# Kernel optimization log

Measured on AMD Instinct MI355X. Metric: run time of the kernel, lower is better.

Reference implementation:

```python
import jax, jax.numpy as jnp
import numpy as np

B, S, D, H = 2, 2048, 4096, 32
Dh = D // H          # 128, rotary_dim == head_dim
BASE = 10000.0       # rope_theta
SCALE = Dh ** -0.5


def setup_inputs() -> dict:
    key = jax.random.key(0)
    k0, k1, k2 = jax.random.split(key, 3)
    w_scale = 0.02
    return {
        "hidden_states": jax.random.normal(k0, (B, S, D), jnp.float32),
        "positions": jnp.broadcast_to(jnp.arange(S, dtype=jnp.int32), (B, S)),
        "Wqkv": jax.random.normal(k1, (D, 3 * D), jnp.float32) * w_scale,
        "bqkv": jnp.zeros((3 * D,), jnp.float32),
        "Wproj": jax.random.normal(k2, (D, D), jnp.float32) * w_scale,
    }


def _apply_rope(x, positions):
    # x: [B, S, H, Dh]; neox-style (rotate-half) RoPE, as in vLLM PagedAttentionWithRoPE
    half = Dh // 2
    inv_freq = 1.0 / (BASE ** (jnp.arange(half, dtype=jnp.float32) / half))
    ang = positions[..., None].astype(jnp.float32) * inv_freq      # [B, S, half]
    cos = jnp.cos(ang)[:, :, None, :]                              # [B, S, 1, half]
    sin = jnp.sin(ang)[:, :, None, :]
    x1, x2 = x[..., :half], x[..., half:]
    return jnp.concatenate([x1 * cos - x2 * sin, x2 * cos + x1 * sin], axis=-1)


def reference(hidden_states, positions, Wqkv, bqkv, Wproj):
    # c_attn: fused QKV projection
    qkv = hidden_states @ Wqkv + bqkv                              # [B, S, 3D]
    q, k, v = jnp.split(qkv, 3, axis=-1)
    q = q.reshape(B, S, H, Dh)
    k = k.reshape(B, S, H, Dh)
    v = v.reshape(B, S, H, Dh)
    # fused RoPE on q and k at the given positions
    q = _apply_rope(q, positions)
    k = _apply_rope(k, positions)
    # causal scaled-dot-product attention (prefill semantics of paged attention)
    scores = jnp.einsum("bqhd,bkhd->bhqk", q, k) * SCALE           # [B, H, S, S]
    causal = jnp.tril(jnp.ones((S, S), dtype=bool))
    scores = jnp.where(causal, scores, jnp.finfo(scores.dtype).min)
    attn = jax.nn.softmax(scores, axis=-1)
    ctx = jnp.einsum("bhqk,bkhd->bqhd", attn, v).reshape(B, S, D)
    # c_proj (no bias)
    return ctx @ Wproj
```

## Files before the change

kernel.cpp:

```cpp
#include <hip/hip_runtime.h>

typedef __attribute__((ext_vector_type(8))) short short8;
typedef __attribute__((ext_vector_type(4))) short short4v;
typedef __attribute__((ext_vector_type(4))) float f32x4;

#define LDS8(base, off) (*(const short8*)((const char*)(base) + (off)))
#define GLOAD_LDS16(gp, lp) __builtin_amdgcn_global_load_lds( \
    (const __attribute__((address_space(1))) unsigned int*)(gp), \
    (__attribute__((address_space(3))) unsigned int*)(lp), 16, 0, 0)
#define SBAR() __builtin_amdgcn_s_barrier()
#define SB0() __builtin_amdgcn_sched_barrier(0)

__device__ __forceinline__ short f2bf(float f) {
    unsigned u = __builtin_bit_cast(unsigned, f);
    unsigned r = (u + 0x7FFFu + ((u >> 16) & 1u)) >> 16;
    return (short)r;
}
__device__ __forceinline__ float bf2f(short s) {
    unsigned u = ((unsigned)(unsigned short)s) << 16;
    return __builtin_bit_cast(float, u);
}

__global__ __launch_bounds__(256) void cvt_f32_bf16(const float* __restrict__ in,
                                                    short* __restrict__ out, int n8) {
    int i = blockIdx.x * 256 + threadIdx.x;
    if (i < n8) {
        const f32x4* p = (const f32x4*)(in + (size_t)i * 8);
        f32x4 a = p[0], bq = p[1];
        short8 o;
        o[0] = f2bf(a[0]); o[1] = f2bf(a[1]); o[2] = f2bf(a[2]); o[3] = f2bf(a[3]);
        o[4] = f2bf(bq[0]); o[5] = f2bf(bq[1]); o[6] = f2bf(bq[2]); o[7] = f2bf(bq[3]);
        *(short8*)(out + (size_t)i * 8) = o;
    }
}

__global__ __launch_bounds__(256) void transpose_cvt(const float* __restrict__ W,
                                                     short* __restrict__ Out, int R, int C,
                                                     int permqk) {
    __shared__ float tile[64][33];
    int c0 = blockIdx.x * 64, r0 = blockIdx.y * 32;
    int tid = threadIdx.x;
    int cc4 = (tid & 15) * 4;
#pragma unroll
    for (int it = 0; it < 2; ++it) {
        int rr = (tid >> 4) + it * 16;
        f32x4 v = *(const f32x4*)&W[(size_t)(r0 + rr) * C + c0 + cc4];
#pragma unroll
        for (int i = 0; i < 4; ++i) tile[cc4 + i][rr] = v[i];
    }
    __syncthreads();
    int cc = tid >> 2, r8 = (tid & 3) * 8;
    short8 o;
#pragma unroll
    for (int i = 0; i < 8; ++i) o[i] = f2bf(tile[cc][r8 + i]);
    int orow = c0 + cc;
    if (permqk && orow < 8192) {
        int j = orow & 127;
        int jp = (j < 64) ? (j << 1) : (((j - 64) << 1) | 1);
        orow = (orow & ~127) | jp;
    }
    *(short8*)&Out[(size_t)orow * R + r0 + r8] = o;
}

__global__ __launch_bounds__(256) void rope_table(float* __restrict__ ctab, float* __restrict__ stab) {
    int idx = blockIdx.x * 256 + threadIdx.x;
    int t = idx >> 6, j = idx & 63;
    float inv = expf(-(float)j * (9.210340371976184f / 64.0f));
    float ang = (float)t * inv;
    ctab[idx] = cosf(ang);
    stab[idx] = sinf(ang);
}

__global__ __launch_bounds__(512, 2) void gemm256(const short* __restrict__ A,
                                                  const short* __restrict__ Bt,
                                                  const float* __restrict__ bias,
                                                  float* __restrict__ Cf,
                                                  int M, int N, int K, int nN,
                                                  const int* __restrict__ pos,
                                                  const float* __restrict__ ctab,
                                                  const float* __restrict__ stab,
                                                  short* __restrict__ Qr,
                                                  short* __restrict__ Kr,
                                                  short* __restrict__ Vtt,
                                                  int mode) {
    __shared__ __align__(16) char smem[131072];
    const int tid = threadIdx.x;
    const int l = tid & 63, w = tid >> 6;
    const int m = l & 15, g = l >> 4, m7 = m & 7;
    const int wm = w >> 2, wn = w & 3;

    int cpx = gridDim.x >> 3;
    int wg = (blockIdx.x & 7) * cpx + (blockIdx.x >> 3);
    int gsz = nN << 3;
    int grp = wg / gsz, rem = wg - grp * gsz;
    int bm = (grp << 3) + (rem & 7);
    int bn = rem >> 3;
    int m0 = bm << 8, n0 = bn << 8;

    const int srow = l >> 3;
    const int sgcol = ((l & 7) ^ srow) << 3;
    const int NT = K >> 6;

    const int AbaseR = wm << 14;
    const int BbaseR = 32768 + ((wn >> 1) << 14);
    const int brow0 = (wn & 1) << 6;

    f32x4 acc[8][4];
    const f32x4 fz = {0.f, 0.f, 0.f, 0.f};
#pragma unroll
    for (int i = 0; i < 8; ++i)
#pragma unroll
        for (int j = 0; j < 4; ++j) acc[i][j] = fz;

    auto stage_half = [&](const short* G, int grow0, int kcol, int ldsoff) {
        GLOAD_LDS16(G + (size_t)(grow0 +      w * 8 + srow) * K + kcol + sgcol,
                    smem + ldsoff + w * 1024);
        GLOAD_LDS16(G + (size_t)(grow0 + 64 + w * 8 + srow) * K + kcol + sgcol,
                    smem + ldsoff + 8192 + w * 1024);
    };

    short8 afX[2][2], afY[2][2], bf[4][2];

#define RD_AF(DST, BASE, I0)                                                     \
    _Pragma("unroll")                                                            \
    for (int i2 = 0; i2 < 2; ++i2) {                                             \
        _Pragma("unroll")                                                        \
        for (int kk = 0; kk < 2; ++kk)                                           \
            DST[i2][kk] = LDS8(BASE, (((I0) + i2) * 16 + m) * 128 + (((kk * 4 + g) ^ m7) << 4)); \
    }
#define RD_BF(BASE)                                                              \
    _Pragma("unroll")                                                            \
    for (int j2 = 0; j2 < 4; ++j2) {                                             \
        _Pragma("unroll")                                                        \
        for (int kk = 0; kk < 2; ++kk)                                           \
            bf[j2][kk] = LDS8(BASE, (brow0 + j2 * 16 + m) * 128 + (((kk * 4 + g) ^ m7) << 4)); \
    }
#define MFMA_IP(IP, AF)                                                          \
    do {                                                                         \
        __builtin_amdgcn_s_setprio(1);                                           \
        _Pragma("unroll")                                                        \
        for (int kk = 0; kk < 2; ++kk) {                                         \
            _Pragma("unroll")                                                    \
            for (int i2 = 0; i2 < 2; ++i2) {                                     \
                _Pragma("unroll")                                                \
                for (int j2 = 0; j2 < 4; ++j2) {                                 \
                    acc[(IP) * 2 + i2][j2] = __builtin_amdgcn_mfma_f32_16x16x32_bf16( \
                        AF[i2][kk], bf[j2][kk], acc[(IP) * 2 + i2][j2], 0, 0, 0); \
                }                                                                \
            }                                                                    \
        }                                                                        \
        __builtin_amdgcn_s_setprio(0);                                           \
    } while (0)

#pragma unroll
    for (int t = 0; t < 2; ++t) {
        int sb = t << 16;
        stage_half(A,  m0,       t * 64, sb);
        stage_half(A,  m0 + 128, t * 64, sb + 16384);
        stage_half(Bt, n0,       t * 64, sb + 32768);
        stage_half(Bt, n0 + 128, t * 64, sb + 49152);
    }
    asm volatile("s_waitcnt vmcnt(8)");
    SB0();
    SBAR();
    {
        const char* Ab0 = smem + AbaseR;
        const char* Bb0 = smem + BbaseR;
        RD_BF(Bb0);
        RD_AF(afX, Ab0, 0);
        SB0();
    }

    for (int kt = 0; kt < NT; ++kt) {
        const int slotb  = (kt & 1) << 16;
        const int slotbN = ((kt + 1) & 1) << 16;
        const char* Ab  = smem + slotb + AbaseR;
        const char* AbN = smem + slotbN + AbaseR;
        const char* BbN = smem + slotbN + BbaseR;
        const bool nx = (kt + 1) < NT;
        const bool pf = (kt + 2) < NT;
        const int kc = (kt + 2) << 6;

        RD_AF(afY, Ab, 2); SB0();
        asm volatile("s_waitcnt lgkmcnt(4)"); SB0();
        MFMA_IP(0, afX);
        RD_AF(afX, Ab, 4); SB0();
        asm volatile("s_waitcnt lgkmcnt(4)"); SB0();
        MFMA_IP(1, afY);
        RD_AF(afY, Ab, 6); SB0();
        asm volatile("s_waitcnt lgkmcnt(4)"); SB0();
        MFMA_IP(2, afX);
        asm volatile("s_waitcnt lgkmcnt(0)"); SB0();
        asm volatile("s_waitcnt vmcnt(0)"); SB0();
        SBAR();
        MFMA_IP(3, afY);
        if (nx) {
            RD_BF(BbN); SB0();
            RD_AF(afX, AbN, 0); SB0();
            if (pf) {
                stage_half(A,  m0,       kc, slotb);
                stage_half(A,  m0 + 128, kc, slotb + 16384);
                stage_half(Bt, n0,       kc, slotb + 32768);
                stage_half(Bt, n0 + 128, kc, slotb + 49152);
            }
        }
    }
#undef RD_AF
#undef RD_BF
#undef MFMA_IP

    if (mode == 0) {
#pragma unroll
        for (int i = 0; i < 8; ++i) {
#pragma unroll
            for (int j = 0; j < 4; ++j) {
#pragma unroll
                for (int r = 0; r < 4; ++r) {
                    int row = m0 + wm * 128 + i * 16 + g * 4 + r;
                    int col = n0 + wn * 64 + j * 16 + m;
                    Cf[(size_t)row * N + col] = acc[i][j][r];
                }
            }
        }
        return;
    }

    int region = n0 >> 12;
    if (region < 2) {
        short* Dst = (region == 0) ? Qr : Kr;
#pragma unroll
        for (int i = 0; i < 8; ++i) {
#pragma unroll
            for (int j = 0; j < 4; ++j) {
                int col = n0 + wn * 64 + j * 16 + m;
                int cr = col & 4095;
                int hh = cr >> 7;
                int jp = cr & 127;
                int jj = jp >> 1;
                int odd = jp & 1;
                int jo = jj + (odd ? 64 : 0);
                float bv = bias ? bias[region * 4096 + hh * 128 + jo] : 0.f;
#pragma unroll
                for (int r = 0; r < 4; ++r) {
                    int row = m0 + wm * 128 + i * 16 + g * 4 + r;
                    float v = acc[i][j][r] + bv;
                    float partner = __shfl_xor(v, 1, 64);
                    int p = pos[row];
                    float c = ctab[p * 64 + jj], si = stab[p * 64 + jj];
                    float outv = odd ? (v * c + partner * si) : (v * c - partner * si);
                    int bI = row >> 11, s = row & 2047;
                    Dst[((size_t)(bI * 32 + hh) * 2048 + s) * 128 + jo] = f2bf(outv);
                }
            }
        }
    } else {
#pragma unroll
        for (int i = 0; i < 8; ++i) {
#pragma unroll
            for (int j = 0; j < 4; ++j) {
                int col = n0 + wn * 64 + j * 16 + m;
                int cr = col & 4095;
                int hh = cr >> 7;
                int d = cr & 127;
                float bv = bias ? bias[8192 + cr] : 0.f;
                int row0 = m0 + wm * 128 + i * 16 + g * 4;
                int bI = row0 >> 11, s0 = row0 & 2047;
                short4v o4;
#pragma unroll
                for (int r = 0; r < 4; ++r) o4[r] = f2bf(acc[i][j][r] + bv);
                *(short4v*)&Vtt[((size_t)(bI * 32 + hh) * 128 + d) * 2048 + s0] = o4;
            }
        }
    }
}

__global__ __launch_bounds__(512, 4) void flash_fwd(const short* __restrict__ Q,
                                                    const short* __restrict__ Kt,
                                                    const short* __restrict__ Vt,
                                                    short* __restrict__ ctx) {
    const int S = 2048;
    const float SCALE = 0.08838834764831845f;
    __shared__ __align__(16) char smem[65536];

    int tid = threadIdx.x, l = tid & 63, w = tid >> 6;
    int m = l & 15, g = l >> 4, m7 = m & 7;
    int qg = blockIdx.x, h = blockIdx.y, b = blockIdx.z;
    int bh = b * 32 + h;
    int q0 = qg * 128 + w * 16;

    const short* Qg = Q + ((size_t)bh * S + q0) * 128;
    const short* Kg = Kt + (size_t)bh * S * 128;
    const short* Vg = Vt + (size_t)bh * 128 * S;

    short8 qf[4];
#pragma unroll
    for (int kb = 0; kb < 4; ++kb)
        qf[kb] = *(const short8*)(Qg + m * 128 + kb * 32 + g * 8);

    const f32x4 fz = {0.f, 0.f, 0.f, 0.f};
    f32x4 O[8];
#pragma unroll
    for (int nb = 0; nb < 8; ++nb) O[nb] = fz;
    f32x4 La = fz;
    short8 ones;
#pragma unroll
    for (int i = 0; i < 8; ++i) ones[i] = (short)0x3F80;

    const short* Kp[2]; const short* Vp[2]; int KlO[2], VlO[2];
#pragma unroll
    for (int q = 0; q < 2; ++q) {
        int c = w * 2 + q;
        int rowK = c * 4 + (l >> 4);
        Kp[q] = Kg + (size_t)rowK * 128 + (((l & 15) ^ (rowK & 7)) * 8);
        KlO[q] = c * 1024;
        int rowV = c * 8 + (l >> 3);
        Vp[q] = Vg + (size_t)rowV * S + (((l & 7) ^ (rowV & 7)) * 8);
        VlO[q] = c * 1024;
    }

    auto stageK = [&](int t, int slot) {
#pragma unroll
        for (int q = 0; q < 2; ++q)
            GLOAD_LDS16(Kp[q] + (size_t)t * 8192, smem + slot * 16384 + KlO[q]);
    };
    auto stageV = [&](int t) {
#pragma unroll
        for (int q = 0; q < 2; ++q)
            GLOAD_LDS16(Vp[q] + t * 64, smem + 32768 + VlO[q]);
    };

    int nkt = 2 * qg + 2;
    stageK(0, 0);
    stageV(0);

    for (int kt = 0; kt < nkt; ++kt) {
        int slot = kt & 1;
        const char* Kl = smem + slot * 16384;
        const char* Vl = smem + 32768;
        char* Pl = smem + 49152 + w * 2048;
        int k0 = kt * 64;
        bool comp = (k0 <= q0 + 15);
        bool more = (kt + 1 < nkt);

        if (more) { stageK(kt + 1, slot ^ 1); asm volatile("s_waitcnt vmcnt(4)"); }
        else      {                           asm volatile("s_waitcnt vmcnt(2)"); }
        SB0();
        SBAR();
        if (comp) {
            f32x4 sc[4];
#pragma unroll
            for (int j = 0; j < 4; ++j) sc[j] = fz;
#pragma unroll
            for (int kb = 0; kb < 4; ++kb) {
#pragma unroll
                for (int j = 0; j < 4; ++j) {
                    short8 kf = LDS8(Kl, (j * 16 + m) * 256 + (((kb * 4 + g) ^ m7) << 4));
                    sc[j] = __builtin_amdgcn_mfma_f32_16x16x32_bf16(qf[kb], kf, sc[j], 0, 0, 0);
                }
            }
            bool diag = (k0 + 63 > q0);
#pragma unroll
            for (int r = 0; r < 4; ++r) {
                int qrow = q0 + g * 4 + r;
                float s0 = sc[0][r] * SCALE;
                float s1 = sc[1][r] * SCALE;
                float s2 = sc[2][r] * SCALE;
                float s3 = sc[3][r] * SCALE;
                if (diag) {
                    if (k0 + m > qrow)      s0 = -__builtin_inff();
                    if (k0 + 16 + m > qrow) s1 = -__builtin_inff();
                    if (k0 + 32 + m > qrow) s2 = -__builtin_inff();
                    if (k0 + 48 + m > qrow) s3 = -__builtin_inff();
                }
                float p0 = __expf(s0);
                float p1 = __expf(s1);
                float p2 = __expf(s2);
                float p3 = __expf(s3);
                int pr = g * 4 + r;
                char* pw = Pl + pr * 128;
                float pv[4] = {p0, p1, p2, p3};
#pragma unroll
                for (int j = 0; j < 4; ++j) {
                    int lb = j * 32 + m * 2;
                    int pb = (((lb >> 4) ^ (pr & 7)) << 4) | (lb & 15);
                    *(short*)(pw + pb) = f2bf(pv[j]);
                }
            }
        }
        if (more) asm volatile("s_waitcnt vmcnt(2)");
        else      asm volatile("s_waitcnt vmcnt(0)");
        SB0();
        SBAR();
        if (comp) {
            short8 pf[2];
#pragma unroll
            for (int kh = 0; kh < 2; ++kh)
                pf[kh] = LDS8(Pl, m * 128 + (((kh * 4 + g) ^ m7) << 4));
#pragma unroll
            for (int kh = 0; kh < 2; ++kh) {
                La = __builtin_amdgcn_mfma_f32_16x16x32_bf16(pf[kh], ones, La, 0, 0, 0);
#pragma unroll
                for (int nb = 0; nb < 8; ++nb) {
                    int d = nb * 16 + m;
                    short8 vf = LDS8(Vl, d * 128 + (((kh * 4 + g) ^ m7) << 4));
                    O[nb] = __builtin_amdgcn_mfma_f32_16x16x32_bf16(pf[kh], vf, O[nb], 0, 0, 0);
                }
            }
        }
        SBAR();
        if (more) stageV(kt + 1);
    }
#pragma unroll
    for (int nb = 0; nb < 8; ++nb) {
#pragma unroll
        for (int r = 0; r < 4; ++r) {
            int row = q0 + g * 4 + r;
            float v = O[nb][r] / La[r];
            ctx[(size_t)(b * S + row) * 4096 + h * 128 + nb * 16 + m] = f2bf(v);
        }
    }
}

extern "C" void kernel_launch(void* const* d_in, const int* in_sizes, int n_in,
                              void* d_out, int out_size, void* d_ws, size_t ws_size,
                              hipStream_t stream) {
    const float* hidden    = (const float*)d_in[0];
    const int*   positions = (const int*)d_in[1];
    const float* Wqkv      = (const float*)d_in[2];
    const float* bqkv      = (const float*)d_in[3];
    const float* Wproj     = (const float*)d_in[4];
    float* out = (float*)d_out;
    char* ws = (char*)d_ws;

    short* Abf    = (short*)(ws + 0ull);
    short* WqkvT  = (short*)(ws + 33554432ull);
    short* WprojT = (short*)(ws + 134217728ull);
    short* Qr     = (short*)(ws + 268435456ull);
    short* Kr     = (short*)(ws + 301989888ull);
    short* Vt     = (short*)(ws + 335544320ull);
    short* ctx    = (short*)(ws + 369098752ull);
    float* ctab   = (float*)(ws + 402653184ull);
    float* stab   = (float*)(ws + 403177472ull);

    cvt_f32_bf16<<<8192, 256, 0, stream>>>(hidden, Abf, 2097152);
    transpose_cvt<<<dim3(192, 128), 256, 0, stream>>>(Wqkv, WqkvT, 4096, 12288, 1);
    transpose_cvt<<<dim3(64, 128), 256, 0, stream>>>(Wproj, WprojT, 4096, 4096, 0);
    rope_table<<<512, 256, 0, stream>>>(ctab, stab);
    gemm256<<<dim3(768), 512, 0, stream>>>(Abf, WqkvT, bqkv, nullptr, 4096, 12288, 4096, 48,
                                           positions, ctab, stab, Qr, Kr, Vt, 1);
    flash_fwd<<<dim3(16, 32, 2), 512, 0, stream>>>(Qr, Kr, Vt, ctx);
    gemm256<<<dim3(256), 512, 0, stream>>>(ctx, WprojT, nullptr, out, 4096, 4096, 4096, 16,
                                           nullptr, nullptr, nullptr, nullptr, nullptr, nullptr, 0);
}
```

Baseline: 757.5 us.

## Replace double-buffered LDS pipeline in GEMM with single-buffered load-then-compute loop

```diff
diff --git a/kernel.cpp b/kernel.cpp
--- a/kernel.cpp
+++ b/kernel.cpp
@@ -83,7 +83,7 @@
                                                   short* __restrict__ Kr,
                                                   short* __restrict__ Vtt,
                                                   int mode) {
-    __shared__ __align__(16) char smem[131072];
+    __shared__ __align__(16) char smem[65536];
     const int tid = threadIdx.x;
     const int l = tid & 63, w = tid >> 6;
     const int m = l & 15, g = l >> 4, m7 = m & 7;
@@ -118,22 +118,30 @@
         GLOAD_LDS16(G + (size_t)(grow0 + 64 + w * 8 + srow) * K + kcol + sgcol,
                     smem + ldsoff + 8192 + w * 1024);
     };
+    auto stage_tile = [&](int kcol) {
+        stage_half(A,  m0,       kcol, 0);
+        stage_half(A,  m0 + 128, kcol, 16384);
+        stage_half(Bt, n0,       kcol, 32768);
+        stage_half(Bt, n0 + 128, kcol, 49152);
+    };
 
     short8 afX[2][2], afY[2][2], bf[4][2];
-
-#define RD_AF(DST, BASE, I0)                                                     \
+    const char* Ab = smem + AbaseR;
+    const char* Bb = smem + BbaseR;
+
+#define RD_AF(DST, I0)                                                           \
     _Pragma("unroll")                                                            \
     for (int i2 = 0; i2 < 2; ++i2) {                                             \
         _Pragma("unroll")                                                        \
         for (int kk = 0; kk < 2; ++kk)                                           \
-            DST[i2][kk] = LDS8(BASE, (((I0) + i2) * 16 + m) * 128 + (((kk * 4 + g) ^ m7) << 4)); \
-    }
-#define RD_BF(BASE)                                                              \
+            DST[i2][kk] = LDS8(Ab, (((I0) + i2) * 16 + m) * 128 + (((kk * 4 + g) ^ m7) << 4)); \
+    }
+#define RD_BF()                                                                  \
     _Pragma("unroll")                                                            \
     for (int j2 = 0; j2 < 4; ++j2) {                                             \
         _Pragma("unroll")                                                        \
         for (int kk = 0; kk < 2; ++kk)                                           \
-            bf[j2][kk] = LDS8(BASE, (brow0 + j2 * 16 + m) * 128 + (((kk * 4 + g) ^ m7) << 4)); \
+            bf[j2][kk] = LDS8(Bb, (brow0 + j2 * 16 + m) * 128 + (((kk * 4 + g) ^ m7) << 4)); \
     }
 #define MFMA_IP(IP, AF)                                                          \
     do {                                                                         \
@@ -152,57 +160,39 @@
         __builtin_amdgcn_s_setprio(0);                                           \
     } while (0)
 
-#pragma unroll
-    for (int t = 0; t < 2; ++t) {
-        int sb = t << 16;
-        stage_half(A,  m0,       t * 64, sb);
-        stage_half(A,  m0 + 128, t * 64, sb + 16384);
-        stage_half(Bt, n0,       t * 64, sb + 32768);
-        stage_half(Bt, n0 + 128, t * 64, sb + 49152);
-    }
-    asm volatile("s_waitcnt vmcnt(8)");
+    stage_tile(0);
+    asm volatile("s_waitcnt vmcnt(0)");
     SB0();
     SBAR();
-    {
-        const char* Ab0 = smem + AbaseR;
-        const char* Bb0 = smem + BbaseR;
-        RD_BF(Bb0);
-        RD_AF(afX, Ab0, 0);
-        SB0();
-    }
 
     for (int kt = 0; kt < NT; ++kt) {
-        const int slotb  = (kt & 1) << 16;
-        const int slotbN = ((kt + 1) & 1) << 16;
-        const char* Ab  = smem + slotb + AbaseR;
-        const char* AbN = smem + slotbN + AbaseR;
-        const char* BbN = smem + slotbN + BbaseR;
-        const bool nx = (kt + 1) < NT;
-        const bool pf = (kt + 2) < NT;
-        const int kc = (kt + 2) << 6;
-
-        RD_AF(afY, Ab, 2); SB0();
-        asm volatile("s_waitcnt lgkmcnt(4)"); SB0();
+        RD_BF();
+        RD_AF(afX, 0);
+        RD_AF(afY, 2);
+        SB0();
+        asm volatile("s_waitcnt lgkmcnt(4)");
+        SB0();
         MFMA_IP(0, afX);
-        RD_AF(afX, Ab, 4); SB0();
-        asm volatile("s_waitcnt lgkmcnt(4)"); SB0();
+        RD_AF(afX, 4);
+        SB0();
+        asm volatile("s_waitcnt lgkmcnt(4)");
+        SB0();
         MFMA_IP(1, afY);
-        RD_AF(afY, Ab, 6); SB0();
-        asm volatile("s_waitcnt lgkmcnt(4)"); SB0();
+        RD_AF(afY, 6);
+        SB0();
+        asm volatile("s_waitcnt lgkmcnt(4)");
+        SB0();
         MFMA_IP(2, afX);
-        asm volatile("s_waitcnt lgkmcnt(0)"); SB0();
-        asm volatile("s_waitcnt vmcnt(0)"); SB0();
+        asm volatile("s_waitcnt lgkmcnt(0)");
+        SB0();
+        MFMA_IP(3, afY);
+
         SBAR();
-        MFMA_IP(3, afY);
-        if (nx) {
-            RD_BF(BbN); SB0();
-            RD_AF(afX, AbN, 0); SB0();
-            if (pf) {
-                stage_half(A,  m0,       kc, slotb);
-                stage_half(A,  m0 + 128, kc, slotb + 16384);
-                stage_half(Bt, n0,       kc, slotb + 32768);
-                stage_half(Bt, n0 + 128, kc, slotb + 49152);
-            }
+        if (kt + 1 < NT) {
+            stage_tile((kt + 1) << 6);
+            asm volatile("s_waitcnt vmcnt(0)");
+            SB0();
+            SBAR();
         }
     }
 #undef RD_AF
```

New measurement: 969.7 us. 28.0% more time.
